# Performance work log

Measured on AMD Instinct MI355X. Metric: run time of the kernel, lower is better.

## Reference

```python
import jax, jax.numpy as jnp
import numpy as np

N, E, F, H, O, G = 100000, 1600000, 128, 128, 64, 1024


def _prelu(x, a):
    return jnp.where(x >= 0, x, a * x)


def _gcn_conv(h, src, dst, w, W, b, n_nodes):
    # GCNConv with scalar edge weights and weight-1 self loops.
    deg = jax.ops.segment_sum(w, dst, num_segments=n_nodes) + 1.0  # [N]
    dis = jax.lax.rsqrt(deg)                                       # deg^-1/2
    hW = h @ W.T                                                   # [N,H]
    coef = (w * dis[src] * dis[dst])[:, None]                      # [E,1]
    agg = jax.ops.segment_sum(hW[src] * coef, dst, num_segments=n_nodes)
    agg = agg + hW * (1.0 / deg)[:, None]                          # self loops
    return agg + b


def setup_inputs() -> dict:
    key = jax.random.key(0)
    ks = jax.random.split(key, 12)
    x = jax.random.normal(ks[0], (N, F), dtype=jnp.float32)
    edge_index = jax.random.randint(ks[1], (2, E), 0, N, dtype=jnp.int64)
    edge_attr = jax.random.uniform(ks[2], (E,), dtype=jnp.float32)
    batch = jnp.sort(jax.random.randint(ks[3], (N,), 0, G, dtype=jnp.int64))
    s = lambda fan_in: 1.0 / np.sqrt(fan_in)
    fc1_w = jax.random.uniform(ks[4], (H, F), jnp.float32, -s(F), s(F))
    fc1_b = jax.random.uniform(ks[5], (H,), jnp.float32, -s(F), s(F))
    gc1_w = jax.random.uniform(ks[6], (H, H), jnp.float32, -s(H), s(H))
    gc1_b = jnp.zeros((H,), jnp.float32)
    gc2_w = jax.random.uniform(ks[7], (H, H), jnp.float32, -s(H), s(H))
    gc2_b = jnp.zeros((H,), jnp.float32)
    fc2_w = jax.random.uniform(ks[8], (O, H), jnp.float32, -s(H), s(H))
    fc2_b = jax.random.uniform(ks[9], (O,), jnp.float32, -s(H), s(H))
    a_fc1 = jnp.float32(0.25)
    a_gc1 = jnp.float32(0.25)
    a_gc2 = jnp.float32(0.25)
    return dict(x=x, edge_index=edge_index, edge_attr=edge_attr, batch=batch,
                fc1_w=fc1_w, fc1_b=fc1_b, gc1_w=gc1_w, gc1_b=gc1_b,
                gc2_w=gc2_w, gc2_b=gc2_b, fc2_w=fc2_w, fc2_b=fc2_b,
                a_fc1=a_fc1, a_gc1=a_gc1, a_gc2=a_gc2)


def reference(x, edge_index, edge_attr, batch, fc1_w, fc1_b, gc1_w, gc1_b,
              gc2_w, gc2_b, fc2_w, fc2_b, a_fc1, a_gc1, a_gc2):
    n_nodes = x.shape[0]
    src, dst = edge_index[0], edge_index[1]
    h = _prelu(x @ fc1_w.T + fc1_b, a_fc1)
    h = _prelu(_gcn_conv(h, src, dst, edge_attr, gc1_w, gc1_b, n_nodes), a_gc1)
    h = _prelu(_gcn_conv(h, src, dst, edge_attr, gc2_w, gc2_b, n_nodes), a_gc2)
    # global mean pool over graphs
    sums = jax.ops.segment_sum(h, batch, num_segments=G)
    cnt = jax.ops.segment_sum(jnp.ones((n_nodes,), h.dtype), batch, num_segments=G)
    hg = sums / jnp.maximum(cnt, 1.0)[:, None]
    # L2 normalize (torch normalize, eps=1e-12)
    hg = hg / jnp.maximum(jnp.linalg.norm(hg, axis=1, keepdims=True), 1e-12)
    return hg @ fc2_w.T + fc2_b
```

## Files before the change

### kernel.cpp

```cpp
#include <hip/hip_runtime.h>
#include <hip/hip_fp16.h>


#define CHK 1024
typedef unsigned int u32;
using f16 = _Float16;
using f16x8 = __attribute__((ext_vector_type(8))) _Float16;
using f32x4 = __attribute__((ext_vector_type(4))) float;

__global__ __launch_bounds__(256) void k_hist(const int* __restrict__ dst,
                                              const float* __restrict__ w,
                                              int* __restrict__ cnt,
                                              float* __restrict__ degf, int E) {
  int e = blockIdx.x * 256 + threadIdx.x;
  if (e < E) {
    int d = dst[e];
    atomicAdd(&cnt[d], 1);
    atomicAdd(&degf[d], w[e]);
  }
}

__global__ __launch_bounds__(256) void k_dis(const float* __restrict__ degf,
                                             float* __restrict__ dis,
                                             float* __restrict__ inv, int N) {
  int n = blockIdx.x * 256 + threadIdx.x;
  if (n < N) {
    float deg = degf[n] + 1.0f;
    dis[n] = rsqrtf(deg);
    inv[n] = 1.0f / deg;
  }
}

__global__ __launch_bounds__(256) void k_scan_reduce(const int* __restrict__ cnt,
                                                     int* __restrict__ chunkSum, int N) {
  __shared__ int sd[256];
  int b = blockIdx.x, t = threadIdx.x;
  int base = b * CHK + t * 4;
  int s = 0;
#pragma unroll
  for (int i = 0; i < 4; i++)
    if (base + i < N) s += cnt[base + i];
  sd[t] = s;
  __syncthreads();
  for (int off = 128; off; off >>= 1) {
    if (t < off) sd[t] += sd[t + off];
    __syncthreads();
  }
  if (t == 0) chunkSum[b] = sd[0];
}

__global__ void k_scan_chunks(const int* __restrict__ chunkSum,
                              int* __restrict__ chunkOff, int NC) {
  if (threadIdx.x == 0 && blockIdx.x == 0) {
    int s = 0;
    for (int i = 0; i < NC; i++) {
      chunkOff[i] = s;
      s += chunkSum[i];
    }
  }
}

__global__ __launch_bounds__(256) void k_scan_final(const int* __restrict__ cnt,
                                                    const int* __restrict__ chunkOff,
                                                    int* __restrict__ rowptr,
                                                    int* __restrict__ cursor, int N, int E) {
  __shared__ int sd[256];
  int b = blockIdx.x, t = threadIdx.x;
  int base = b * CHK + t * 4;
  int v[4], loc[4];
#pragma unroll
  for (int i = 0; i < 4; i++) v[i] = (base + i < N) ? cnt[base + i] : 0;
  loc[0] = 0;
  loc[1] = v[0];
  loc[2] = v[0] + v[1];
  loc[3] = v[0] + v[1] + v[2];
  int tot = loc[3] + v[3];
  sd[t] = tot;
  __syncthreads();
  for (int off = 1; off < 256; off <<= 1) {
    int xv = (t >= off) ? sd[t - off] : 0;
    __syncthreads();
    sd[t] += xv;
    __syncthreads();
  }
  int tbase = (t ? sd[t - 1] : 0) + chunkOff[b];
#pragma unroll
  for (int i = 0; i < 4; i++) {
    if (base + i < N) {
      int r = tbase + loc[i];
      rowptr[base + i] = r;
      cursor[base + i] = r;
    }
  }
  if (b == 0 && t == 0) rowptr[N] = E;
}

__global__ __launch_bounds__(256) void k_scatter(const int* __restrict__ src,
                                                 const int* __restrict__ dst,
                                                 const float* __restrict__ w,
                                                 const float* __restrict__ dis,
                                                 int* __restrict__ cursor,
                                                 int2* __restrict__ csr, int E) {
  int e = blockIdx.x * 256 + threadIdx.x;
  if (e < E) {
    int s = src[e], d = dst[e];
    float c = w[e] * dis[s] * dis[d];
    int p = atomicAdd(&cursor[d], 1);
    int2 v;
    v.x = s;
    v.y = __float_as_int(c);
    csr[p] = v;
  }
}

__global__ __launch_bounds__(256) void k_prep_bfrag(const float* __restrict__ W,
                                                    f16x8* __restrict__ Bf) {
  int t = blockIdx.x * 256 + threadIdx.x;
  int combo = t >> 6;
  int l = t & 63;
  int o = (combo & 7) * 16 + (l & 15);
  int k0 = (combo >> 3) * 32 + (l >> 4) * 8;
  f16x8 b;
#pragma unroll
  for (int i = 0; i < 8; i++) b[i] = (f16)W[o * 128 + k0 + i];
  Bf[combo * 64 + l] = b;
}

template <bool FP32_IN, bool BIAS>
__global__ __launch_bounds__(256) void k_gemm_mfma(const f16* __restrict__ Ah,
                                                   const float* __restrict__ Af,
                                                   const f16x8* __restrict__ Bf,
                                                   f16* __restrict__ out,
                                                   const float* __restrict__ bias,
                                                   const float* __restrict__ slope,
                                                   int N) {
  __shared__ f16 ls[64 * 128];
  int t = threadIdx.x;
  int w = t >> 6, l = t & 63;
  int l15 = l & 15, kgrp = l >> 4;
  int nodeBase = blockIdx.x * 64 + w * 16;
  f32x4 acc[8];
#pragma unroll
  for (int ct = 0; ct < 8; ct++)
#pragma unroll
    for (int j = 0; j < 4; j++) acc[ct][j] = 0.f;

  int arow = nodeBase + l15;
  if (arow >= N) arow = N - 1;
#pragma unroll
  for (int kc = 0; kc < 4; kc++) {
    f16x8 a;
    if (FP32_IN) {
      const float4* p0 = (const float4*)(Af + (size_t)arow * 128 + kc * 32 + kgrp * 8);
      float4 x0 = p0[0], x1 = p0[1];
      a[0] = (f16)x0.x; a[1] = (f16)x0.y; a[2] = (f16)x0.z; a[3] = (f16)x0.w;
      a[4] = (f16)x1.x; a[5] = (f16)x1.y; a[6] = (f16)x1.z; a[7] = (f16)x1.w;
    } else {
      a = *(const f16x8*)(Ah + (size_t)arow * 128 + kc * 32 + kgrp * 8);
    }
#pragma unroll
    for (int ct = 0; ct < 8; ct++) {
      f16x8 b = Bf[(kc * 8 + ct) * 64 + l];
      acc[ct] = __builtin_amdgcn_mfma_f32_16x16x32_f16(a, b, acc[ct], 0, 0, 0);
    }
  }
  float sl = BIAS ? *slope : 0.f;
  f16* slab = ls + w * 16 * 128;
#pragma unroll
  for (int ct = 0; ct < 8; ct++) {
    float bv = BIAS ? bias[ct * 16 + l15] : 0.f;
#pragma unroll
    for (int j = 0; j < 4; j++) {
      float v = acc[ct][j];
      if (BIAS) {
        v += bv;
        v = v >= 0.f ? v : sl * v;
      }
      slab[(kgrp * 4 + j) * 128 + ct * 16 + l15] = (f16)v;
    }
  }
  __syncthreads();
  {
    int r = l >> 2;
    int gnode = nodeBase + r;
    if (gnode < N) {
      const uint4* srcp = (const uint4*)(slab + r * 128);
      uint4* dstp = (uint4*)(out + (size_t)gnode * 128);
#pragma unroll
      for (int i = 0; i < 4; i++) {
        int chunk = (l & 3) + i * 4;
        dstp[chunk] = srcp[chunk];
      }
    }
  }
}

template <bool POOL>
__global__ __launch_bounds__(256) void k_agg_h(const __half2* __restrict__ hW,
                                               const int* __restrict__ rowptr,
                                               const int2* __restrict__ csr,
                                               const float* __restrict__ inv,
                                               const float* __restrict__ bias,
                                               const float* __restrict__ slope,
                                               const int* __restrict__ batch,
                                               __half2* __restrict__ outh,
                                               float* __restrict__ pool,
                                               float* __restrict__ cntg, int N) {
  int wid = (blockIdx.x * 256 + threadIdx.x) >> 6;
  if (wid >= N) return;
  int l = threadIdx.x & 63;
  int r0 = rowptr[wid], r1 = rowptr[wid + 1];
  float2 acc;
  {
    float2 f = __half22float2(hW[(size_t)wid * 64 + l]);
    float iv = inv[wid];
    acc.x = f.x * iv;
    acc.y = f.y * iv;
  }
  for (int base = r0; base < r1; base += 64) {
    int idx = base + l;
    int sl = 0;
    float cl = 0.f;
    if (idx < r1) {
      int2 e = csr[idx];
      sl = e.x;
      cl = __int_as_float(e.y);
    }
    int m = min(64, r1 - base);
    for (int k = 0; k < m; k += 16) {
      __half2 v[16];
      float c[16];
#pragma unroll
      for (int i = 0; i < 16; i++) {
        int s = __shfl(sl, k + i);
        c[i] = __shfl(cl, k + i);
        v[i] = hW[(size_t)s * 64 + l];
      }
#pragma unroll
      for (int i = 0; i < 16; i++) {
        float2 f = __half22float2(v[i]);
        acc.x += f.x * c[i];
        acc.y += f.y * c[i];
      }
    }
  }
  float a = *slope;
  float2 b = *(const float2*)&bias[l * 2];
  acc.x += b.x;
  acc.y += b.y;
  acc.x = acc.x >= 0.f ? acc.x : a * acc.x;
  acc.y = acc.y >= 0.f ? acc.y : a * acc.y;
  if (POOL) {
    int g = batch[wid];
    atomicAdd(&pool[(size_t)g * 128 + l * 2], acc.x);
    atomicAdd(&pool[(size_t)g * 128 + l * 2 + 1], acc.y);
    if (l == 0) atomicAdd(&cntg[g], 1.0f);
  } else {
    outh[(size_t)wid * 64 + l] = __float22half2_rn(acc);
  }
}

__global__ __launch_bounds__(64) void k_final(const float* __restrict__ pool,
                                              const float* __restrict__ cntg,
                                              const float* __restrict__ fc2w,
                                              const float* __restrict__ fc2b,
                                              float* __restrict__ out) {
  __shared__ float hg[128];
  int g = blockIdx.x, l = threadIdx.x;
  float cnt = cntg[g];
  float ic = 1.0f / fmaxf(cnt, 1.0f);
  float2 v = *(const float2*)&pool[(size_t)g * 128 + l * 2];
  v.x *= ic;
  v.y *= ic;
  float ss = v.x * v.x + v.y * v.y;
#pragma unroll
  for (int off = 1; off < 64; off <<= 1) ss += __shfl_xor(ss, off);
  float nrm = sqrtf(ss);
  float sc = 1.0f / fmaxf(nrm, 1e-12f);
  hg[l * 2] = v.x * sc;
  hg[l * 2 + 1] = v.y * sc;
  __syncthreads();
  float acc = fc2b[l];
#pragma unroll 4
  for (int k = 0; k < 128; k++) acc += hg[k] * fc2w[l * 128 + k];
  out[(size_t)g * 64 + l] = acc;
}

extern "C" void kernel_launch(void* const* d_in, const int* in_sizes, int n_in,
                              void* d_out, int out_size, void* d_ws, size_t ws_size,
                              hipStream_t stream) {
  const float* x = (const float*)d_in[0];
  const int* ei = (const int*)d_in[1];
  const float* ew = (const float*)d_in[2];
  const int* batch = (const int*)d_in[3];
  const float* fc1_w = (const float*)d_in[4];
  const float* fc1_b = (const float*)d_in[5];
  const float* gc1_w = (const float*)d_in[6];
  const float* gc1_b = (const float*)d_in[7];
  const float* gc2_w = (const float*)d_in[8];
  const float* gc2_b = (const float*)d_in[9];
  const float* fc2_w = (const float*)d_in[10];
  const float* fc2_b = (const float*)d_in[11];
  const float* a_fc1 = (const float*)d_in[12];
  const float* a_gc1 = (const float*)d_in[13];
  const float* a_gc2 = (const float*)d_in[14];

  int N = in_sizes[0] / 128;
  int E = in_sizes[2];
  int G = out_size / 64;
  const int* src = ei;
  const int* dst = ei + E;

  char* p = (char*)d_ws;
  auto carve = [&](size_t bytes) -> char* {
    char* r = p;
    p += (bytes + 255) & ~(size_t)255;
    return r;
  };
  f16* bufA = (f16*)carve((size_t)N * 128 * 2);
  f16* bufH = (f16*)carve((size_t)N * 128 * 2);
  int2* csr = (int2*)carve((size_t)E * 8);
  int* cnt = (int*)carve((size_t)N * 4);
  int* rowptr = (int*)carve((size_t)(N + 1) * 4);
  int* cursor = (int*)carve((size_t)N * 4);
  float* degf = (float*)carve((size_t)N * 4);
  float* dis = (float*)carve((size_t)N * 4);
  float* inv = (float*)carve((size_t)N * 4);
  f16x8* Bf1 = (f16x8*)carve(2048 * 16);
  f16x8* Bf2 = (f16x8*)carve(2048 * 16);
  f16x8* Bf3 = (f16x8*)carve(2048 * 16);
  int NC = (N + CHK - 1) / CHK;
  int* chunkSum = (int*)carve((size_t)NC * 4);
  int* chunkOff = (int*)carve((size_t)NC * 4);
  float* pool = (float*)carve((size_t)G * 128 * 4);
  float* cntg = (float*)carve((size_t)G * 4);

  hipMemsetAsync(cnt, 0, (size_t)N * 4, stream);
  hipMemsetAsync(degf, 0, (size_t)N * 4, stream);
  hipMemsetAsync(pool, 0, (size_t)G * 128 * 4, stream);
  hipMemsetAsync(cntg, 0, (size_t)G * 4, stream);

  k_prep_bfrag<<<8, 256, 0, stream>>>(fc1_w, Bf1);
  k_prep_bfrag<<<8, 256, 0, stream>>>(gc1_w, Bf2);
  k_prep_bfrag<<<8, 256, 0, stream>>>(gc2_w, Bf3);

  int gE = (E + 255) / 256;
  int gN = (N + 255) / 256;
  k_hist<<<gE, 256, 0, stream>>>(dst, ew, cnt, degf, E);
  k_dis<<<gN, 256, 0, stream>>>(degf, dis, inv, N);
  k_scan_reduce<<<NC, 256, 0, stream>>>(cnt, chunkSum, N);
  k_scan_chunks<<<1, 64, 0, stream>>>(chunkSum, chunkOff, NC);
  k_scan_final<<<NC, 256, 0, stream>>>(cnt, chunkOff, rowptr, cursor, N, E);
  k_scatter<<<gE, 256, 0, stream>>>(src, dst, ew, dis, cursor, csr, E);

  int gGemm = (N + 63) / 64;
  int gAgg = (int)(((size_t)N * 64 + 255) / 256);

  k_gemm_mfma<true, true><<<gGemm, 256, 0, stream>>>(nullptr, x, Bf1, bufA, fc1_b, a_fc1, N);
  k_gemm_mfma<false, false><<<gGemm, 256, 0, stream>>>(bufA, nullptr, Bf2, bufH, nullptr, nullptr, N);
  k_agg_h<false><<<gAgg, 256, 0, stream>>>((const __half2*)bufH, rowptr, csr, inv, gc1_b,
                                           a_gc1, batch, (__half2*)bufA, nullptr, cntg, N);
  k_gemm_mfma<false, false><<<gGemm, 256, 0, stream>>>(bufA, nullptr, Bf3, bufH, nullptr, nullptr, N);
  k_agg_h<true><<<gAgg, 256, 0, stream>>>((const __half2*)bufH, rowptr, csr, inv, gc2_b,
                                          a_gc2, batch, nullptr, pool, cntg, N);
  k_final<<<G, 64, 0, stream>>>(pool, cntg, fc2_w, fc2_b, (float*)d_out);
}
```

Baseline: 607.5 us.

## Bucket edges by destination chunk and source range, aggregate via LDS atomics

Edges are bucketed by 128-node destination chunk and one of 8 source ranges, with the local destination packed into the source index. Each block accumulates its bucket into an LDS tile using shared-memory atomics, so gathers hit a narrower source window with better cache locality. A separate reduce kernel then sums the 8 fp16 partial buffers and applies the self loop, bias and PReLU, plus pooling on the second layer. The cost is an 8x N x 128 fp16 partial buffer (about 200MB of writes and reads per layer), LDS atomic contention, and extra fp16 rounding of the partials. There is a fallback to the old CSR path when workspace is too small.

```diff
diff --git a/kernel.cpp b/kernel.cpp
--- a/kernel.cpp
+++ b/kernel.cpp
@@ -8,16 +8,12 @@
 using f16x8 = __attribute__((ext_vector_type(8))) _Float16;
 using f32x4 = __attribute__((ext_vector_type(4))) float;
 
-__global__ __launch_bounds__(256) void k_hist(const int* __restrict__ dst,
-                                              const float* __restrict__ w,
-                                              int* __restrict__ cnt,
-                                              float* __restrict__ degf, int E) {
+
+__global__ __launch_bounds__(256) void k_hist_deg(const int* __restrict__ dst,
+                                                  const float* __restrict__ w,
+                                                  float* __restrict__ degf, int E) {
   int e = blockIdx.x * 256 + threadIdx.x;
-  if (e < E) {
-    int d = dst[e];
-    atomicAdd(&cnt[d], 1);
-    atomicAdd(&degf[d], w[e]);
-  }
+  if (e < E) atomicAdd(&degf[dst[e]], w[e]);
 }
 
 __global__ __launch_bounds__(256) void k_dis(const float* __restrict__ degf,
@@ -29,6 +25,24 @@
     dis[n] = rsqrtf(deg);
     inv[n] = 1.0f / deg;
   }
+}
+
+
+__global__ __launch_bounds__(256) void k_hist_cnt_bucket(const int* __restrict__ src,
+                                                         const int* __restrict__ dst,
+                                                         int* __restrict__ cnt, int E,
+                                                         int RANGE) {
+  int e = blockIdx.x * 256 + threadIdx.x;
+  if (e < E) {
+    int bucket = (dst[e] >> 7) * 8 + (src[e] / RANGE);
+    atomicAdd(&cnt[bucket], 1);
+  }
+}
+
+__global__ __launch_bounds__(256) void k_hist_cnt_dst(const int* __restrict__ dst,
+                                                      int* __restrict__ cnt, int E) {
+  int e = blockIdx.x * 256 + threadIdx.x;
+  if (e < E) atomicAdd(&cnt[dst[e]], 1);
 }
 
 __global__ __launch_bounds__(256) void k_scan_reduce(const int* __restrict__ cnt,
@@ -95,12 +109,33 @@
   if (b == 0 && t == 0) rowptr[N] = E;
 }
 
-__global__ __launch_bounds__(256) void k_scatter(const int* __restrict__ src,
-                                                 const int* __restrict__ dst,
-                                                 const float* __restrict__ w,
-                                                 const float* __restrict__ dis,
-                                                 int* __restrict__ cursor,
-                                                 int2* __restrict__ csr, int E) {
+
+__global__ __launch_bounds__(256) void k_scatter_b(const int* __restrict__ src,
+                                                   const int* __restrict__ dst,
+                                                   const float* __restrict__ w,
+                                                   const float* __restrict__ dis,
+                                                   int* __restrict__ cursor,
+                                                   int2* __restrict__ recs, int E,
+                                                   int RANGE) {
+  int e = blockIdx.x * 256 + threadIdx.x;
+  if (e < E) {
+    int s = src[e], d = dst[e];
+    float c = w[e] * dis[s] * dis[d];
+    int bucket = (d >> 7) * 8 + (s / RANGE);
+    int p = atomicAdd(&cursor[bucket], 1);
+    int2 v;
+    v.x = s | ((d & 127) << 17);
+    v.y = __float_as_int(c);
+    recs[p] = v;
+  }
+}
+
+__global__ __launch_bounds__(256) void k_scatter_d(const int* __restrict__ src,
+                                                   const int* __restrict__ dst,
+                                                   const float* __restrict__ w,
+                                                   const float* __restrict__ dis,
+                                                   int* __restrict__ cursor,
+                                                   int2* __restrict__ csr, int E) {
   int e = blockIdx.x * 256 + threadIdx.x;
   if (e < E) {
     int s = src[e], d = dst[e];
@@ -112,6 +147,7 @@
     csr[p] = v;
   }
 }
+
 
 __global__ __launch_bounds__(256) void k_prep_bfrag(const float* __restrict__ W,
                                                     f16x8* __restrict__ Bf) {
@@ -194,6 +230,110 @@
     }
   }
 }
+
+
+#define LDSTRIDE 132
+
+__global__ __launch_bounds__(256, 2) void k_agg_lds(const __half2* __restrict__ hW,
+                                                    const int* __restrict__ brow,
+                                                    const int2* __restrict__ recs,
+                                                    __half2* __restrict__ P, int N) {
+  extern __shared__ float lds[];
+  int t = threadIdx.x;
+  int bid = blockIdx.x;
+  int r = bid & 7;
+  int chunkBase = (bid >> 3) * 128;
+  for (int i = t; i < 128 * LDSTRIDE / 4; i += 256) ((float4*)lds)[i] = float4{0, 0, 0, 0};
+  __syncthreads();
+
+  int w = t >> 6, l = t & 63;
+  int b0 = brow[bid], b1 = brow[bid + 1];
+  for (int g0 = b0 + w * 64; g0 < b1; g0 += 256) {
+    int idx = g0 + l;
+    int xv = 0;
+    float cv = 0.f;
+    if (idx < b1) {
+      int2 e = recs[idx];
+      xv = e.x;
+      cv = __int_as_float(e.y);
+    }
+    int m = min(64, b1 - g0);
+    for (int k = 0; k < m; k += 16) {
+      __half2 v[16];
+      float cc[16];
+      int dd[16];
+#pragma unroll
+      for (int i = 0; i < 16; i++) {
+        int x = __shfl(xv, k + i);
+        cc[i] = __shfl(cv, k + i);
+        int s = x & 0x1FFFF;
+        dd[i] = (x >> 17) & 127;
+        v[i] = hW[(size_t)s * 64 + l];
+      }
+#pragma unroll
+      for (int i = 0; i < 16; i++) {
+        float2 f = __half22float2(v[i]);
+        float* lp = lds + dd[i] * LDSTRIDE + 2 * l;
+        atomicAdd(lp, f.x * cc[i]);
+        atomicAdd(lp + 1, f.y * cc[i]);
+      }
+    }
+  }
+  __syncthreads();
+  for (int i = 0; i < 8; i++) {
+    int u4 = t + 256 * i;
+    int row = u4 >> 4, pos = u4 & 15;
+    int node = chunkBase + row;
+    if (node < N) {
+      const float* rp = lds + row * LDSTRIDE + pos * 8;
+      __half2 h[4];
+#pragma unroll
+      for (int j = 0; j < 4; j++) h[j] = __float22half2_rn(make_float2(rp[2 * j], rp[2 * j + 1]));
+      *(uint4*)(P + ((size_t)r * N + node) * 64 + pos * 4) = *(uint4*)h;
+    }
+  }
+}
+
+template <bool POOL>
+__global__ __launch_bounds__(256) void k_reduce(const __half2* __restrict__ P,
+                                                const __half2* __restrict__ hW,
+                                                const float* __restrict__ inv,
+                                                const float* __restrict__ bias,
+                                                const float* __restrict__ slope,
+                                                const int* __restrict__ batch,
+                                                __half2* __restrict__ outh,
+                                                float* __restrict__ pool,
+                                                float* __restrict__ cntg, int N) {
+  int i = blockIdx.x * 256 + threadIdx.x;
+  if (i >= N * 64) return;
+  int fp = i & 63;
+  int node = i >> 6;
+  float iv = inv[node];
+  float2 f = __half22float2(hW[i]);
+  float2 acc = make_float2(f.x * iv, f.y * iv);
+  size_t stride = (size_t)N * 64;
+#pragma unroll
+  for (int r = 0; r < 8; r++) {
+    float2 p = __half22float2(P[(size_t)r * stride + i]);
+    acc.x += p.x;
+    acc.y += p.y;
+  }
+  float a = *slope;
+  float2 b = *(const float2*)&bias[fp * 2];
+  acc.x += b.x;
+  acc.y += b.y;
+  acc.x = acc.x >= 0.f ? acc.x : a * acc.x;
+  acc.y = acc.y >= 0.f ? acc.y : a * acc.y;
+  if (POOL) {
+    int g = batch[node];
+    atomicAdd(&pool[(size_t)g * 128 + fp * 2], acc.x);
+    atomicAdd(&pool[(size_t)g * 128 + fp * 2 + 1], acc.y);
+    if (fp == 0) atomicAdd(&cntg[g], 1.0f);
+  } else {
+    outh[i] = __float22half2_rn(acc);
+  }
+}
+
 
 template <bool POOL>
 __global__ __launch_bounds__(256) void k_agg_h(const __half2* __restrict__ hW,
@@ -260,6 +400,7 @@
   }
 }
 
+
 __global__ __launch_bounds__(64) void k_final(const float* __restrict__ pool,
                                               const float* __restrict__ cntg,
                                               const float* __restrict__ fc2w,
@@ -311,6 +452,11 @@
   const int* src = ei;
   const int* dst = ei + E;
 
+  int RANGE = (N + 7) / 8;
+  int NCHUNK = (N + 127) >> 7;
+  int NB = NCHUNK * 8;
+  int NBIG = N > NB ? N : NB;
+
   char* p = (char*)d_ws;
   auto carve = [&](size_t bytes) -> char* {
     char* r = p;
@@ -319,23 +465,25 @@
   };
   f16* bufA = (f16*)carve((size_t)N * 128 * 2);
   f16* bufH = (f16*)carve((size_t)N * 128 * 2);
-  int2* csr = (int2*)carve((size_t)E * 8);
-  int* cnt = (int*)carve((size_t)N * 4);
-  int* rowptr = (int*)carve((size_t)(N + 1) * 4);
-  int* cursor = (int*)carve((size_t)N * 4);
+  int2* recs = (int2*)carve((size_t)E * 8);
+  int* cnt = (int*)carve((size_t)(NBIG + 1) * 4);
+  int* rowptr = (int*)carve((size_t)(NBIG + 1) * 4);
+  int* cursor = (int*)carve((size_t)(NBIG + 1) * 4);
   float* degf = (float*)carve((size_t)N * 4);
   float* dis = (float*)carve((size_t)N * 4);
   float* inv = (float*)carve((size_t)N * 4);
   f16x8* Bf1 = (f16x8*)carve(2048 * 16);
   f16x8* Bf2 = (f16x8*)carve(2048 * 16);
   f16x8* Bf3 = (f16x8*)carve(2048 * 16);
-  int NC = (N + CHK - 1) / CHK;
-  int* chunkSum = (int*)carve((size_t)NC * 4);
-  int* chunkOff = (int*)carve((size_t)NC * 4);
+  int NCmax = (NBIG + CHK - 1) / CHK;
+  int* chunkSum = (int*)carve((size_t)NCmax * 4);
+  int* chunkOff = (int*)carve((size_t)NCmax * 4);
   float* pool = (float*)carve((size_t)G * 128 * 4);
   float* cntg = (float*)carve((size_t)G * 4);
-
-  hipMemsetAsync(cnt, 0, (size_t)N * 4, stream);
+  __half2* partial = (__half2*)carve((size_t)8 * N * 128 * 2);
+  bool useNew = ((size_t)(p - (char*)d_ws) <= ws_size);
+
+  hipMemsetAsync(cnt, 0, (size_t)NBIG * 4, stream);
   hipMemsetAsync(degf, 0, (size_t)N * 4, stream);
   hipMemsetAsync(pool, 0, (size_t)G * 128 * 4, stream);
   hipMemsetAsync(cntg, 0, (size_t)G * 4, stream);
@@ -346,22 +494,47 @@
 
   int gE = (E + 255) / 256;
   int gN = (N + 255) / 256;
-  k_hist<<<gE, 256, 0, stream>>>(dst, ew, cnt, degf, E);
+  k_hist_deg<<<gE, 256, 0, stream>>>(dst, ew, degf, E);
   k_dis<<<gN, 256, 0, stream>>>(degf, dis, inv, N);
-  k_scan_reduce<<<NC, 256, 0, stream>>>(cnt, chunkSum, N);
-  k_scan_chunks<<<1, 64, 0, stream>>>(chunkSum, chunkOff, NC);
-  k_scan_final<<<NC, 256, 0, stream>>>(cnt, chunkOff, rowptr, cursor, N, E);
-  k_scatter<<<gE, 256, 0, stream>>>(src, dst, ew, dis, cursor, csr, E);
+
+  if (useNew) {
+    int NCb = (NB + CHK - 1) / CHK;
+    k_hist_cnt_bucket<<<gE, 256, 0, stream>>>(src, dst, cnt, E, RANGE);
+    k_scan_reduce<<<NCb, 256, 0, stream>>>(cnt, chunkSum, NB);
+    k_scan_chunks<<<1, 64, 0, stream>>>(chunkSum, chunkOff, NCb);
+    k_scan_final<<<NCb, 256, 0, stream>>>(cnt, chunkOff, rowptr, cursor, NB, E);
+    k_scatter_b<<<gE, 256, 0, stream>>>(src, dst, ew, dis, cursor, recs, E, RANGE);
+  } else {
+    int NCn = (N + CHK - 1) / CHK;
+    k_hist_cnt_dst<<<gE, 256, 0, stream>>>(dst, cnt, E);
+    k_scan_reduce<<<NCn, 256, 0, stream>>>(cnt, chunkSum, N);
+    k_scan_chunks<<<1, 64, 0, stream>>>(chunkSum, chunkOff, NCn);
+    k_scan_final<<<NCn, 256, 0, stream>>>(cnt, chunkOff, rowptr, cursor, N, E);
+    k_scatter_d<<<gE, 256, 0, stream>>>(src, dst, ew, dis, cursor, recs, E);
+  }
 
   int gGemm = (N + 63) / 64;
-  int gAgg = (int)(((size_t)N * 64 + 255) / 256);
+  int gElem = (int)(((size_t)N * 64 + 255) / 256);
+  size_t ldsB = 128 * LDSTRIDE * 4;
 
   k_gemm_mfma<true, true><<<gGemm, 256, 0, stream>>>(nullptr, x, Bf1, bufA, fc1_b, a_fc1, N);
   k_gemm_mfma<false, false><<<gGemm, 256, 0, stream>>>(bufA, nullptr, Bf2, bufH, nullptr, nullptr, N);
-  k_agg_h<false><<<gAgg, 256, 0, stream>>>((const __half2*)bufH, rowptr, csr, inv, gc1_b,
-                                           a_gc1, batch, (__half2*)bufA, nullptr, cntg, N);
+  if (useNew) {
+    k_agg_lds<<<NB, 256, ldsB, stream>>>((const __half2*)bufH, rowptr, recs, partial, N);
+    k_reduce<false><<<gElem, 256, 0, stream>>>(partial, (const __half2*)bufH, inv, gc1_b,
+                                               a_gc1, batch, (__half2*)bufA, nullptr, cntg, N);
+  } else {
+    k_agg_h<false><<<gElem, 256, 0, stream>>>((const __half2*)bufH, rowptr, recs, inv, gc1_b,
+                                              a_gc1, batch, (__half2*)bufA, nullptr, cntg, N);
+  }
   k_gemm_mfma<false, false><<<gGemm, 256, 0, stream>>>(bufA, nullptr, Bf3, bufH, nullptr, nullptr, N);
-  k_agg_h<true><<<gAgg, 256, 0, stream>>>((const __half2*)bufH, rowptr, csr, inv, gc2_b,
-                                          a_gc2, batch, nullptr, pool, cntg, N);
+  if (useNew) {
+    k_agg_lds<<<NB, 256, ldsB, stream>>>((const __half2*)bufH, rowptr, recs, partial, N);
+    k_reduce<true><<<gElem, 256, 0, stream>>>(partial, (const __half2*)bufH, inv, gc2_b,
+                                              a_gc2, batch, nullptr, pool, cntg, N);
+  } else {
+    k_agg_h<true><<<gElem, 256, 0, stream>>>((const __half2*)bufH, rowptr, recs, inv, gc2_b,
+                                             a_gc2, batch, nullptr, pool, cntg, N);
+  }
   k_final<<<G, 64, 0, stream>>>(pool, cntg, fc2_w, fc2_b, (float*)d_out);
 }
```

Measured after the change: 613.3 us. Within noise of the previous version (+0.9%).
